# Optimization experiments

Hardware: AMD Instinct MI355X
Metric: run time of the kernel (lower is better)

Reference implementation:

```python
import jax, jax.numpy as jnp
import numpy as np

B, S, H = 2, 2048, 2048      # batch, seq_len, hidden_size
E, K, I = 64, 8, 768         # num_experts, top_k, moe_intermediate_size


def setup_inputs() -> dict:
    key = jax.random.key(0)
    k0, k1, k2, k3, k4 = jax.random.split(key, 5)
    hidden_states = jax.random.normal(k0, (B, S, H), dtype=jnp.float32)
    gate_weight = jax.random.normal(k1, (E, H), dtype=jnp.float32) * 0.02   # router
    w_gate = jax.random.normal(k2, (E, H, I), dtype=jnp.float32) * 0.02    # gate_proj
    w_up = jax.random.normal(k3, (E, H, I), dtype=jnp.float32) * 0.02      # up_proj
    w_down = jax.random.normal(k4, (E, I, H), dtype=jnp.float32) * 0.02    # down_proj
    return {"hidden_states": hidden_states, "gate_weight": gate_weight,
            "w_gate": w_gate, "w_up": w_up, "w_down": w_down}


def _moe_forward(hidden_states, gate_weight, w_gate, w_up, w_down):
    b, s, h = hidden_states.shape
    x = hidden_states.reshape(-1, h)                       # [T, H]
    # ---- router: linear + softmax + top-k + renormalize (fp32, like original) ----
    logits = x.astype(jnp.float32) @ gate_weight.astype(jnp.float32).T  # [T, E]
    scores = jax.nn.softmax(logits, axis=-1)
    topk_w, topk_idx = jax.lax.top_k(scores, K)            # [T, K]
    topk_w = topk_w / jnp.sum(topk_w, axis=-1, keepdims=True)
    # ---- dispatch: replicate each token K times, sort rows by expert id ----
    flat_ids = topk_idx.reshape(-1)                        # [T*K]
    expanded = jnp.repeat(x, K, axis=0)                    # [T*K, H]
    order = jnp.argsort(flat_ids)                          # group rows by expert
    sorted_tokens = expanded[order]                        # [T*K, H], expert-contiguous
    group_sizes = jnp.zeros((E,), jnp.int32).at[flat_ids].add(1)
    # ---- grouped-GEMM expert FFN: down(silu(gate(x)) * up(x)) ----
    g = jax.lax.ragged_dot(sorted_tokens, w_gate, group_sizes)   # [T*K, I]
    u = jax.lax.ragged_dot(sorted_tokens, w_up, group_sizes)     # [T*K, I]
    out = jax.lax.ragged_dot(jax.nn.silu(g) * u, w_down, group_sizes)  # [T*K, H]
    # ---- unshuffle + weighted combine over the K experts per token ----
    inv = jnp.argsort(order)
    outs = out[inv].reshape(-1, K, h)                      # [T, K, H]
    y = jnp.sum(outs * topk_w[:, :, None], axis=1)         # [T, H]
    return y.reshape(b, s, h)


def reference(hidden_states, gate_weight, w_gate, w_up, w_down):
    return _moe_forward(hidden_states, gate_weight, w_gate, w_up, w_down)
```

## Files before the change

### kernel.cpp

```cpp
#include <hip/hip_runtime.h>
#include <math.h>
#include <stdint.h>

constexpr int Bc = 2, Sc = 2048, Hc = 2048, Ec = 64, Kc = 8, Ic = 768;
constexpr int Tc  = Bc * Sc;
constexpr int TKc = Tc * Kc;

__global__ __launch_bounds__(256) void router_topk(
    const float* __restrict__ x, const float* __restrict__ gw,
    int* __restrict__ topk_idx, float* __restrict__ topk_w,
    int* __restrict__ counts)
{
    __shared__ float xs[Hc];
    __shared__ float lg[Ec];
    const int t   = blockIdx.x;
    const int tid = threadIdx.x;

    {
        const float4* src = (const float4*)(x + (size_t)t * Hc);
        float4* dst = (float4*)xs;
        dst[tid * 2]     = src[tid * 2];
        dst[tid * 2 + 1] = src[tid * 2 + 1];
    }
    __syncthreads();

    const int wave = tid >> 6, lane = tid & 63;
    for (int j = 0; j < 16; ++j) {
        const int e = wave * 16 + j;
        const float* gr = gw + (size_t)e * Hc;
        float p = 0.f;
        for (int i = lane; i < Hc; i += 64) p += xs[i] * gr[i];
        for (int off = 32; off; off >>= 1) p += __shfl_down(p, off);
        if (lane == 0) lg[e] = p;
    }
    __syncthreads();

    if (tid < 64) {
        float v = lg[lane];
        int   id = lane;
        float sval[8]; int sid[8];
        for (int k = 0; k < 8; ++k) {
            float bv = v; int bi = id;
            for (int off = 32; off; off >>= 1) {
                float ov = __shfl_down(bv, off);
                int   oi = __shfl_down(bi, off);
                if (ov > bv || (ov == bv && oi < bi)) { bv = ov; bi = oi; }
            }
            bv = __shfl(bv, 0); bi = __shfl(bi, 0);
            sval[k] = bv; sid[k] = bi;
            if (id == bi) v = -INFINITY;
        }
        if (lane == 0) {
            float m = sval[0], s = 0.f, w[8];
            for (int k = 0; k < 8; ++k) { w[k] = expf(sval[k] - m); s += w[k]; }
            const float inv = 1.f / s;
            for (int k = 0; k < 8; ++k) {
                topk_idx[t * 8 + k] = sid[k];
                topk_w[t * 8 + k]   = w[k] * inv;
                atomicAdd(&counts[sid[k]], 1);
            }
        }
    }
}

__global__ void prefix_scan(const int* __restrict__ counts, int* __restrict__ offsets)
{
    if (threadIdx.x == 0 && blockIdx.x == 0) {
        int s = 0;
        for (int e = 0; e < Ec; ++e) { offsets[e] = s; s += counts[e]; }
        offsets[Ec] = s;
    }
}

__global__ __launch_bounds__(256) void scatter_rows(
    const int* __restrict__ topk_idx, const int* __restrict__ offsets,
    int* __restrict__ cursor, int* __restrict__ rowtok)
{
    const int idx = blockIdx.x * 256 + threadIdx.x;
    if (idx < TKc) {
        const int e   = topk_idx[idx];
        const int pos = offsets[e] + atomicAdd(&cursor[e], 1);
        rowtok[pos] = idx;
    }
}

__global__ __launch_bounds__(256) void gemm_act(
    const float* __restrict__ x, const float* __restrict__ wg,
    const float* __restrict__ wu, const int* __restrict__ offsets,
    const int* __restrict__ rowtok, float* __restrict__ act)
{
    __shared__ float As[64][17];
    __shared__ float Bg[16][68];
    __shared__ float Bu[16][68];

    const int e    = blockIdx.y;
    const int base = offsets[e];
    const int M    = offsets[e + 1] - base;
    const int row0 = blockIdx.z * 64;
    if (row0 >= M) return;
    const int n0  = blockIdx.x * 64;
    const int tid = threadIdx.x;

    const int ar = tid >> 2, aq = tid & 3;
    const bool avalid = (row0 + ar) < M;
    const int tok = avalid ? (rowtok[base + row0 + ar] >> 3) : 0;
    const float* arow = x + (size_t)tok * Hc + aq * 4;

    const int bk = tid >> 4, bq = tid & 15;
    const float* wg_base = wg + (size_t)e * Hc * Ic + n0;
    const float* wu_base = wu + (size_t)e * Hc * Ic + n0;

    const int tr = tid >> 4, tc = tid & 15;
    float accg[4][4] = {}, accu[4][4] = {};

    for (int h0 = 0; h0 < Hc; h0 += 16) {
        float4 av = make_float4(0.f, 0.f, 0.f, 0.f);
        if (avalid) av = *(const float4*)(arow + h0);
        As[ar][aq * 4 + 0] = av.x; As[ar][aq * 4 + 1] = av.y;
        As[ar][aq * 4 + 2] = av.z; As[ar][aq * 4 + 3] = av.w;

        const float4 gv = *(const float4*)(wg_base + (size_t)(h0 + bk) * Ic + bq * 4);
        const float4 uv = *(const float4*)(wu_base + (size_t)(h0 + bk) * Ic + bq * 4);
        Bg[bk][bq * 4 + 0] = gv.x; Bg[bk][bq * 4 + 1] = gv.y;
        Bg[bk][bq * 4 + 2] = gv.z; Bg[bk][bq * 4 + 3] = gv.w;
        Bu[bk][bq * 4 + 0] = uv.x; Bu[bk][bq * 4 + 1] = uv.y;
        Bu[bk][bq * 4 + 2] = uv.z; Bu[bk][bq * 4 + 3] = uv.w;
        __syncthreads();

        #pragma unroll
        for (int kk = 0; kk < 16; ++kk) {
            float a[4], bg[4], bu[4];
            #pragma unroll
            for (int i2 = 0; i2 < 4; ++i2) a[i2] = As[tr * 4 + i2][kk];
            #pragma unroll
            for (int j = 0; j < 4; ++j) { bg[j] = Bg[kk][tc * 4 + j]; bu[j] = Bu[kk][tc * 4 + j]; }
            #pragma unroll
            for (int i2 = 0; i2 < 4; ++i2)
                #pragma unroll
                for (int j = 0; j < 4; ++j) {
                    accg[i2][j] += a[i2] * bg[j];
                    accu[i2][j] += a[i2] * bu[j];
                }
        }
        __syncthreads();
    }

    #pragma unroll
    for (int i2 = 0; i2 < 4; ++i2) {
        const int r = tr * 4 + i2;
        if (row0 + r < M) {
            float* orow = act + (size_t)(base + row0 + r) * Ic + n0 + tc * 4;
            #pragma unroll
            for (int j = 0; j < 4; ++j) {
                const float g = accg[i2][j], u = accu[i2][j];
                const float s = g / (1.f + expf(-g));
                orow[j] = s * u;
            }
        }
    }
}

__global__ __launch_bounds__(256) void gemm_down(
    const float* __restrict__ act, const float* __restrict__ wd,
    const int* __restrict__ offsets, const int* __restrict__ rowtok,
    const float* __restrict__ topk_w, float* __restrict__ out)
{
    __shared__ float As[64][17];
    __shared__ float Bs[16][68];

    const int e    = blockIdx.y;
    const int base = offsets[e];
    const int M    = offsets[e + 1] - base;
    const int row0 = blockIdx.z * 64;
    if (row0 >= M) return;
    const int n0  = blockIdx.x * 64;
    const int tid = threadIdx.x;

    const int ar = tid >> 2, aq = tid & 3;
    const bool avalid = (row0 + ar) < M;
    const float* arow = act + (size_t)(base + row0 + ar) * Ic + aq * 4;

    const int bk = tid >> 4, bq = tid & 15;
    const float* wd_base = wd + (size_t)e * Ic * Hc + n0;

    const int tr = tid >> 4, tc = tid & 15;
    float acc[4][4] = {};

    for (int i0 = 0; i0 < Ic; i0 += 16) {
        float4 av = make_float4(0.f, 0.f, 0.f, 0.f);
        if (avalid) av = *(const float4*)(arow + i0);
        As[ar][aq * 4 + 0] = av.x; As[ar][aq * 4 + 1] = av.y;
        As[ar][aq * 4 + 2] = av.z; As[ar][aq * 4 + 3] = av.w;

        const float4 bv = *(const float4*)(wd_base + (size_t)(i0 + bk) * Hc + bq * 4);
        Bs[bk][bq * 4 + 0] = bv.x; Bs[bk][bq * 4 + 1] = bv.y;
        Bs[bk][bq * 4 + 2] = bv.z; Bs[bk][bq * 4 + 3] = bv.w;
        __syncthreads();

        #pragma unroll
        for (int kk = 0; kk < 16; ++kk) {
            float a[4], b[4];
            #pragma unroll
            for (int i2 = 0; i2 < 4; ++i2) a[i2] = As[tr * 4 + i2][kk];
            #pragma unroll
            for (int j = 0; j < 4; ++j) b[j] = Bs[kk][tc * 4 + j];
            #pragma unroll
            for (int i2 = 0; i2 < 4; ++i2)
                #pragma unroll
                for (int j = 0; j < 4; ++j) acc[i2][j] += a[i2] * b[j];
        }
        __syncthreads();
    }

    #pragma unroll
    for (int i2 = 0; i2 < 4; ++i2) {
        const int r = tr * 4 + i2;
        if (row0 + r < M) {
            const int idx = rowtok[base + row0 + r];
            const int t   = idx >> 3;
            const float w = topk_w[idx];
            float* orow = out + (size_t)t * Hc + n0 + tc * 4;
            #pragma unroll
            for (int j = 0; j < 4; ++j) atomicAdd(&orow[j], w * acc[i2][j]);
        }
    }
}

extern "C" void kernel_launch(void* const* d_in, const int* in_sizes, int n_in,
                              void* d_out, int out_size, void* d_ws, size_t ws_size,
                              hipStream_t stream)
{
    const float* x  = (const float*)d_in[0];
    const float* gw = (const float*)d_in[1];
    const float* wg = (const float*)d_in[2];
    const float* wu = (const float*)d_in[3];
    const float* wd = (const float*)d_in[4];
    float* out = (float*)d_out;

    int*   topk_idx = (int*)d_ws;
    float* topk_w   = (float*)(topk_idx + TKc);
    int*   counts   = (int*)(topk_w + TKc);
    int*   offsets  = counts + Ec;
    int*   cursor   = offsets + Ec + 1;
    int*   rowtok   = cursor + Ec;
    float* act      = (float*)((((uintptr_t)(rowtok + TKc)) + 255) & ~(uintptr_t)255);

    hipMemsetAsync(counts, 0, (size_t)(3 * Ec + 1) * sizeof(int), stream);
    hipMemsetAsync(out, 0, (size_t)out_size * sizeof(float), stream);

    router_topk<<<Tc, 256, 0, stream>>>(x, gw, topk_idx, topk_w, counts);
    prefix_scan<<<1, 64, 0, stream>>>(counts, offsets);
    scatter_rows<<<TKc / 256, 256, 0, stream>>>(topk_idx, offsets, cursor, rowtok);
    gemm_act<<<dim3(Ic / 64, Ec, 64), 256, 0, stream>>>(x, wg, wu, offsets, rowtok, act);
    gemm_down<<<dim3(Hc / 64, Ec, 64), 256, 0, stream>>>(act, wd, offsets, rowtok, topk_w, out);
}
```

Baseline: 5.996 ms.

## Run expert GEMMs on bf16 MFMA with hi/lo split emulating fp32

Replaces the scalar-FMA fp32 tiled expert GEMMs with MFMA 16x16x32 bf16 kernels. Each fp32 operand is split into bf16 hi and lo parts, and three MFMAs per tile recover near-fp32 accuracy. Tiles grow to 128x128 and 128x256, LDS is XOR-swizzled, global loads are register double-buffered, and the intermediate activation is stored as a bf16 hi/lo pair. The aim is to move the compute-bound FFN onto the matrix cores, at the cost of on-the-fly weight conversion in every block and a small loss of precision versus true fp32.

Measured after the change: 8.624 ms. 1.44x slower.

```diff
diff --git a/kernel.cpp b/kernel.cpp
--- a/kernel.cpp
+++ b/kernel.cpp
@@ -5,6 +5,31 @@
 constexpr int Bc = 2, Sc = 2048, Hc = 2048, Ec = 64, Kc = 8, Ic = 768;
 constexpr int Tc  = Bc * Sc;
 constexpr int TKc = Tc * Kc;
+
+typedef __attribute__((ext_vector_type(8))) short          bf16x8;
+typedef __attribute__((ext_vector_type(4))) short          s16x4;
+typedef __attribute__((ext_vector_type(8))) unsigned short u16x8;
+typedef __attribute__((ext_vector_type(4))) float          f32x4;
+
+#define SWZ(b) ((b) ^ ((((b) >> 6) & 7) << 4))
+
+__device__ __forceinline__ unsigned short bf_hi(float f) {
+    unsigned u = __float_as_uint(f);
+    u += 0x7fffu + ((u >> 16) & 1u);
+    return (unsigned short)(u >> 16);
+}
+__device__ __forceinline__ void bf_split(float f, short& h, short& l) {
+    unsigned short hb = bf_hi(f);
+    float rem = f - __uint_as_float((unsigned)hb << 16);
+    h = (short)hb;
+    l = (short)bf_hi(rem);
+}
+__device__ __forceinline__ float fc(const float4& v, int j) {
+    switch (j) { case 0: return v.x; case 1: return v.y; case 2: return v.z; default: return v.w; }
+}
+__device__ __forceinline__ f32x4 mma16(bf16x8 a, bf16x8 b, f32x4 c) {
+    return __builtin_amdgcn_mfma_f32_16x16x32_bf16(a, b, c, 0, 0, 0);
+}
 
 __global__ __launch_bounds__(256) void router_topk(
     const float* __restrict__ x, const float* __restrict__ gw,
@@ -84,144 +109,280 @@
     }
 }
 
-__global__ __launch_bounds__(256) void gemm_act(
+__global__ __launch_bounds__(256, 2) void gemm_act(
     const float* __restrict__ x, const float* __restrict__ wg,
     const float* __restrict__ wu, const int* __restrict__ offsets,
-    const int* __restrict__ rowtok, float* __restrict__ act)
-{
-    __shared__ float As[64][17];
-    __shared__ float Bg[16][68];
-    __shared__ float Bu[16][68];
-
-    const int e    = blockIdx.y;
+    const int* __restrict__ rowtok,
+    unsigned short* __restrict__ act_hi, unsigned short* __restrict__ act_lo)
+{
+    __shared__ __align__(16) short Ah[128*32], Al[128*32];
+    __shared__ __align__(16) short Gh[128*32], Gl[128*32];
+    __shared__ __align__(16) short Uh[128*32], Ul[128*32];
+
+    const int e    = blockIdx.z;
     const int base = offsets[e];
     const int M    = offsets[e + 1] - base;
-    const int row0 = blockIdx.z * 64;
+    const int row0 = blockIdx.x * 128;
     if (row0 >= M) return;
-    const int n0  = blockIdx.x * 64;
+    const int n0  = blockIdx.y * 128;
     const int tid = threadIdx.x;
 
-    const int ar = tid >> 2, aq = tid & 3;
-    const bool avalid = (row0 + ar) < M;
-    const int tok = avalid ? (rowtok[base + row0 + ar] >> 3) : 0;
-    const float* arow = x + (size_t)tok * Hc + aq * 4;
-
-    const int bk = tid >> 4, bq = tid & 15;
-    const float* wg_base = wg + (size_t)e * Hc * Ic + n0;
-    const float* wu_base = wu + (size_t)e * Hc * Ic + n0;
-
-    const int tr = tid >> 4, tc = tid & 15;
-    float accg[4][4] = {}, accu[4][4] = {};
-
-    for (int h0 = 0; h0 < Hc; h0 += 16) {
-        float4 av = make_float4(0.f, 0.f, 0.f, 0.f);
-        if (avalid) av = *(const float4*)(arow + h0);
-        As[ar][aq * 4 + 0] = av.x; As[ar][aq * 4 + 1] = av.y;
-        As[ar][aq * 4 + 2] = av.z; As[ar][aq * 4 + 3] = av.w;
-
-        const float4 gv = *(const float4*)(wg_base + (size_t)(h0 + bk) * Ic + bq * 4);
-        const float4 uv = *(const float4*)(wu_base + (size_t)(h0 + bk) * Ic + bq * 4);
-        Bg[bk][bq * 4 + 0] = gv.x; Bg[bk][bq * 4 + 1] = gv.y;
-        Bg[bk][bq * 4 + 2] = gv.z; Bg[bk][bq * 4 + 3] = gv.w;
-        Bu[bk][bq * 4 + 0] = uv.x; Bu[bk][bq * 4 + 1] = uv.y;
-        Bu[bk][bq * 4 + 2] = uv.z; Bu[bk][bq * 4 + 3] = uv.w;
+    const int ar = tid >> 1;
+    const int ak = (tid & 1) * 16;
+    int ridx = base + row0 + ar;
+    if (ridx > TKc - 1) ridx = TKc - 1;
+    const int tok = rowtok[ridx] >> 3;
+    const float* aptr = x + (size_t)tok * Hc + ak;
+
+    const int bq = (tid >> 3) * 4;
+    const int bk = (tid & 7) * 4;
+    const float* gptr = wg + (size_t)e * Hc * Ic + (size_t)bk * Ic + (n0 + bq);
+    const float* uptr = wu + (size_t)e * Hc * Ic + (size_t)bk * Ic + (n0 + bq);
+
+    const int lane = tid & 63, wave = tid >> 6;
+    const int wm = wave >> 1, wn = wave & 1;
+    const int l15 = lane & 15, lk = lane >> 4;
+
+    int aoff[4], boff[4];
+    #pragma unroll
+    for (int m = 0; m < 4; ++m) aoff[m] = SWZ((wm*64 + m*16 + l15) * 64 + lk*16);
+    #pragma unroll
+    for (int n = 0; n < 4; ++n) boff[n] = SWZ((wn*64 + n*16 + l15) * 64 + lk*16);
+
+    f32x4 accg[4][4] = {}, accu[4][4] = {};
+
+    float4 ra[4], rg[4], ru[4];
+    #pragma unroll
+    for (int i = 0; i < 4; ++i) ra[i] = *(const float4*)(aptr + i*4);
+    #pragma unroll
+    for (int i = 0; i < 4; ++i) rg[i] = *(const float4*)(gptr + (size_t)i * Ic);
+    #pragma unroll
+    for (int i = 0; i < 4; ++i) ru[i] = *(const float4*)(uptr + (size_t)i * Ic);
+
+    for (int h0 = 0; h0 < Hc; h0 += 32) {
         __syncthreads();
 
-        #pragma unroll
-        for (int kk = 0; kk < 16; ++kk) {
-            float a[4], bg[4], bu[4];
-            #pragma unroll
-            for (int i2 = 0; i2 < 4; ++i2) a[i2] = As[tr * 4 + i2][kk];
-            #pragma unroll
-            for (int j = 0; j < 4; ++j) { bg[j] = Bg[kk][tc * 4 + j]; bu[j] = Bu[kk][tc * 4 + j]; }
-            #pragma unroll
-            for (int i2 = 0; i2 < 4; ++i2)
+        {
+            const int b0 = ar*64 + ak*2;
+            #pragma unroll
+            for (int q = 0; q < 2; ++q) {
+                bf16x8 vh, vl;
                 #pragma unroll
-                for (int j = 0; j < 4; ++j) {
-                    accg[i2][j] += a[i2] * bg[j];
-                    accu[i2][j] += a[i2] * bu[j];
+                for (int i = 0; i < 2; ++i)
+                    #pragma unroll
+                    for (int j = 0; j < 4; ++j) {
+                        short h, l; bf_split(fc(ra[q*2 + i], j), h, l);
+                        vh[i*4 + j] = h; vl[i*4 + j] = l;
+                    }
+                *(bf16x8*)((char*)Ah + SWZ(b0 + q*16)) = vh;
+                *(bf16x8*)((char*)Al + SWZ(b0 + q*16)) = vl;
+            }
+        }
+        #pragma unroll
+        for (int j = 0; j < 4; ++j) {
+            const int b = (bq + j)*64 + bk*2;
+            s16x4 gh, gl, uh, ul;
+            #pragma unroll
+            for (int i = 0; i < 4; ++i) {
+                short h, l;
+                bf_split(fc(rg[i], j), h, l); gh[i] = h; gl[i] = l;
+                bf_split(fc(ru[i], j), h, l); uh[i] = h; ul[i] = l;
+            }
+            *(s16x4*)((char*)Gh + SWZ(b)) = gh;
+            *(s16x4*)((char*)Gl + SWZ(b)) = gl;
+            *(s16x4*)((char*)Uh + SWZ(b)) = uh;
+            *(s16x4*)((char*)Ul + SWZ(b)) = ul;
+        }
+
+        if (h0 + 32 < Hc) {
+            #pragma unroll
+            for (int i = 0; i < 4; ++i) ra[i] = *(const float4*)(aptr + (h0 + 32) + i*4);
+            #pragma unroll
+            for (int i = 0; i < 4; ++i) rg[i] = *(const float4*)(gptr + (size_t)(h0 + 32 + i) * Ic);
+            #pragma unroll
+            for (int i = 0; i < 4; ++i) ru[i] = *(const float4*)(uptr + (size_t)(h0 + 32 + i) * Ic);
+        }
+
+        __syncthreads();
+
+        bf16x8 fah[4], fal[4];
+        #pragma unroll
+        for (int m = 0; m < 4; ++m) {
+            fah[m] = *(const bf16x8*)((const char*)Ah + aoff[m]);
+            fal[m] = *(const bf16x8*)((const char*)Al + aoff[m]);
+        }
+        #pragma unroll
+        for (int n = 0; n < 4; ++n) {
+            bf16x8 bh = *(const bf16x8*)((const char*)Gh + boff[n]);
+            bf16x8 bl = *(const bf16x8*)((const char*)Gl + boff[n]);
+            #pragma unroll
+            for (int m = 0; m < 4; ++m) {
+                accg[m][n] = mma16(fah[m], bh, accg[m][n]);
+                accg[m][n] = mma16(fal[m], bh, accg[m][n]);
+                accg[m][n] = mma16(fah[m], bl, accg[m][n]);
+            }
+            bh = *(const bf16x8*)((const char*)Uh + boff[n]);
+            bl = *(const bf16x8*)((const char*)Ul + boff[n]);
+            #pragma unroll
+            for (int m = 0; m < 4; ++m) {
+                accu[m][n] = mma16(fah[m], bh, accu[m][n]);
+                accu[m][n] = mma16(fal[m], bh, accu[m][n]);
+                accu[m][n] = mma16(fah[m], bl, accu[m][n]);
+            }
+        }
+    }
+
+    #pragma unroll
+    for (int m = 0; m < 4; ++m) {
+        #pragma unroll
+        for (int r = 0; r < 4; ++r) {
+            const int rl = wm*64 + m*16 + lk*4 + r;
+            if (row0 + rl < M) {
+                unsigned short* oh = act_hi + (size_t)(base + row0 + rl) * Ic + n0;
+                unsigned short* ol = act_lo + (size_t)(base + row0 + rl) * Ic + n0;
+                #pragma unroll
+                for (int n = 0; n < 4; ++n) {
+                    const int c = wn*64 + n*16 + l15;
+                    const float g = accg[m][n][r];
+                    const float u = accu[m][n][r];
+                    const float s = (g / (1.f + expf(-g))) * u;
+                    short h, l; bf_split(s, h, l);
+                    oh[c] = (unsigned short)h;
+                    ol[c] = (unsigned short)l;
                 }
-        }
-        __syncthreads();
-    }
-
-    #pragma unroll
-    for (int i2 = 0; i2 < 4; ++i2) {
-        const int r = tr * 4 + i2;
-        if (row0 + r < M) {
-            float* orow = act + (size_t)(base + row0 + r) * Ic + n0 + tc * 4;
-            #pragma unroll
-            for (int j = 0; j < 4; ++j) {
-                const float g = accg[i2][j], u = accu[i2][j];
-                const float s = g / (1.f + expf(-g));
-                orow[j] = s * u;
-            }
-        }
-    }
-}
-
-__global__ __launch_bounds__(256) void gemm_down(
-    const float* __restrict__ act, const float* __restrict__ wd,
-    const int* __restrict__ offsets, const int* __restrict__ rowtok,
-    const float* __restrict__ topk_w, float* __restrict__ out)
-{
-    __shared__ float As[64][17];
-    __shared__ float Bs[16][68];
-
-    const int e    = blockIdx.y;
+            }
+        }
+    }
+}
+
+__global__ __launch_bounds__(256, 2) void gemm_down(
+    const unsigned short* __restrict__ act_hi, const unsigned short* __restrict__ act_lo,
+    const float* __restrict__ wd, const int* __restrict__ offsets,
+    const int* __restrict__ rowtok, const float* __restrict__ topk_w,
+    float* __restrict__ out)
+{
+    __shared__ __align__(16) short Ah[128*32], Al[128*32];
+    __shared__ __align__(16) short Bh[256*32], Bl[256*32];
+
+    const int e    = blockIdx.z;
     const int base = offsets[e];
     const int M    = offsets[e + 1] - base;
-    const int row0 = blockIdx.z * 64;
+    const int row0 = blockIdx.x * 128;
     if (row0 >= M) return;
-    const int n0  = blockIdx.x * 64;
+    const int n0  = blockIdx.y * 256;
     const int tid = threadIdx.x;
 
-    const int ar = tid >> 2, aq = tid & 3;
-    const bool avalid = (row0 + ar) < M;
-    const float* arow = act + (size_t)(base + row0 + ar) * Ic + aq * 4;
-
-    const int bk = tid >> 4, bq = tid & 15;
-    const float* wd_base = wd + (size_t)e * Ic * Hc + n0;
-
-    const int tr = tid >> 4, tc = tid & 15;
-    float acc[4][4] = {};
-
-    for (int i0 = 0; i0 < Ic; i0 += 16) {
-        float4 av = make_float4(0.f, 0.f, 0.f, 0.f);
-        if (avalid) av = *(const float4*)(arow + i0);
-        As[ar][aq * 4 + 0] = av.x; As[ar][aq * 4 + 1] = av.y;
-        As[ar][aq * 4 + 2] = av.z; As[ar][aq * 4 + 3] = av.w;
-
-        const float4 bv = *(const float4*)(wd_base + (size_t)(i0 + bk) * Hc + bq * 4);
-        Bs[bk][bq * 4 + 0] = bv.x; Bs[bk][bq * 4 + 1] = bv.y;
-        Bs[bk][bq * 4 + 2] = bv.z; Bs[bk][bq * 4 + 3] = bv.w;
+    const int ar = tid >> 1;
+    const int ak = (tid & 1) * 16;
+    int ridx = base + row0 + ar;
+    if (ridx > TKc - 1) ridx = TKc - 1;
+    const unsigned short* ahp = act_hi + (size_t)ridx * Ic + ak;
+    const unsigned short* alp = act_lo + (size_t)ridx * Ic + ak;
+
+    const int bq = (tid >> 3) * 4;
+    const int bk = (tid & 7) * 4;
+    const float* bptr = wd + (size_t)e * Ic * Hc + (size_t)bk * Hc + (n0 + bq);
+
+    const int lane = tid & 63, wave = tid >> 6;
+    const int wm = wave >> 1, wn = wave & 1;
+    const int l15 = lane & 15, lk = lane >> 4;
+
+    int aoff[4], boff[8];
+    #pragma unroll
+    for (int m = 0; m < 4; ++m) aoff[m] = SWZ((wm*64 + m*16 + l15) * 64 + lk*16);
+    #pragma unroll
+    for (int n = 0; n < 8; ++n) boff[n] = SWZ((wn*128 + n*16 + l15) * 64 + lk*16);
+
+    f32x4 acc[4][8] = {};
+
+    u16x8 rah[2], ral[2];
+    float4 rb[2][4];
+    #pragma unroll
+    for (int q = 0; q < 2; ++q) {
+        rah[q] = *(const u16x8*)(ahp + q*8);
+        ral[q] = *(const u16x8*)(alp + q*8);
+    }
+    #pragma unroll
+    for (int p = 0; p < 2; ++p)
+        #pragma unroll
+        for (int i = 0; i < 4; ++i)
+            rb[p][i] = *(const float4*)(bptr + (size_t)i * Hc + p*128);
+
+    for (int i0 = 0; i0 < Ic; i0 += 32) {
         __syncthreads();
 
-        #pragma unroll
-        for (int kk = 0; kk < 16; ++kk) {
-            float a[4], b[4];
-            #pragma unroll
-            for (int i2 = 0; i2 < 4; ++i2) a[i2] = As[tr * 4 + i2][kk];
-            #pragma unroll
-            for (int j = 0; j < 4; ++j) b[j] = Bs[kk][tc * 4 + j];
-            #pragma unroll
-            for (int i2 = 0; i2 < 4; ++i2)
+        {
+            const int b0 = ar*64 + ak*2;
+            *(u16x8*)((char*)Ah + SWZ(b0))      = rah[0];
+            *(u16x8*)((char*)Ah + SWZ(b0 + 16)) = rah[1];
+            *(u16x8*)((char*)Al + SWZ(b0))      = ral[0];
+            *(u16x8*)((char*)Al + SWZ(b0 + 16)) = ral[1];
+        }
+        #pragma unroll
+        for (int p = 0; p < 2; ++p)
+            #pragma unroll
+            for (int j = 0; j < 4; ++j) {
+                const int b = (bq + p*128 + j)*64 + bk*2;
+                s16x4 vh, vl;
                 #pragma unroll
-                for (int j = 0; j < 4; ++j) acc[i2][j] += a[i2] * b[j];
-        }
+                for (int i = 0; i < 4; ++i) {
+                    short h, l; bf_split(fc(rb[p][i], j), h, l);
+                    vh[i] = h; vl[i] = l;
+                }
+                *(s16x4*)((char*)Bh + SWZ(b)) = vh;
+                *(s16x4*)((char*)Bl + SWZ(b)) = vl;
+            }
+
+        if (i0 + 32 < Ic) {
+            #pragma unroll
+            for (int q = 0; q < 2; ++q) {
+                rah[q] = *(const u16x8*)(ahp + (i0 + 32) + q*8);
+                ral[q] = *(const u16x8*)(alp + (i0 + 32) + q*8);
+            }
+            #pragma unroll
+            for (int p = 0; p < 2; ++p)
+                #pragma unroll
+                for (int i = 0; i < 4; ++i)
+                    rb[p][i] = *(const float4*)(bptr + (size_t)(i0 + 32 + i) * Hc + p*128);
+        }
+
         __syncthreads();
-    }
-
-    #pragma unroll
-    for (int i2 = 0; i2 < 4; ++i2) {
-        const int r = tr * 4 + i2;
-        if (row0 + r < M) {
-            const int idx = rowtok[base + row0 + r];
-            const int t   = idx >> 3;
-            const float w = topk_w[idx];
-            float* orow = out + (size_t)t * Hc + n0 + tc * 4;
-            #pragma unroll
-            for (int j = 0; j < 4; ++j) atomicAdd(&orow[j], w * acc[i2][j]);
+
+        bf16x8 fah[4], fal[4];
+        #pragma unroll
+        for (int m = 0; m < 4; ++m) {
+            fah[m] = *(const bf16x8*)((const char*)Ah + aoff[m]);
+            fal[m] = *(const bf16x8*)((const char*)Al + aoff[m]);
+        }
+        #pragma unroll
+        for (int n = 0; n < 8; ++n) {
+            bf16x8 bh = *(const bf16x8*)((const char*)Bh + boff[n]);
+            bf16x8 bl = *(const bf16x8*)((const char*)Bl + boff[n]);
+            #pragma unroll
+            for (int m = 0; m < 4; ++m) {
+                acc[m][n] = mma16(fah[m], bh, acc[m][n]);
+                acc[m][n] = mma16(fal[m], bh, acc[m][n]);
+                acc[m][n] = mma16(fah[m], bl, acc[m][n]);
+            }
+        }
+    }
+
+    #pragma unroll
+    for (int m = 0; m < 4; ++m) {
+        #pragma unroll
+        for (int r = 0; r < 4; ++r) {
+            const int rl = wm*64 + m*16 + lk*4 + r;
+            if (row0 + rl < M) {
+                const int idx = rowtok[base + row0 + rl];
+                const int t   = idx >> 3;
+                const float w = topk_w[idx];
+                float* orow = out + (size_t)t * Hc + n0;
+                #pragma unroll
+                for (int n = 0; n < 8; ++n) {
+                    const int c = wn*128 + n*16 + l15;
+                    atomicAdd(&orow[c], w * acc[m][n][r]);
+                }
+            }
         }
     }
 }
@@ -238,19 +399,20 @@
     float* out = (float*)d_out;
 
     int*   topk_idx = (int*)d_ws;
-    float* topk_w   = (float*)(topk_idx + TKc);
-    int*   counts   = (int*)(topk_w + TKc);
+    float* topk_wv  = (float*)(topk_idx + TKc);
+    int*   counts   = (int*)(topk_wv + TKc);
     int*   offsets  = counts + Ec;
     int*   cursor   = offsets + Ec + 1;
     int*   rowtok   = cursor + Ec;
-    float* act      = (float*)((((uintptr_t)(rowtok + TKc)) + 255) & ~(uintptr_t)255);
+    unsigned short* act_hi = (unsigned short*)((((uintptr_t)(rowtok + TKc)) + 255) & ~(uintptr_t)255);
+    unsigned short* act_lo = act_hi + (size_t)TKc * Ic;
 
     hipMemsetAsync(counts, 0, (size_t)(3 * Ec + 1) * sizeof(int), stream);
     hipMemsetAsync(out, 0, (size_t)out_size * sizeof(float), stream);
 
-    router_topk<<<Tc, 256, 0, stream>>>(x, gw, topk_idx, topk_w, counts);
+    router_topk<<<Tc, 256, 0, stream>>>(x, gw, topk_idx, topk_wv, counts);
     prefix_scan<<<1, 64, 0, stream>>>(counts, offsets);
     scatter_rows<<<TKc / 256, 256, 0, stream>>>(topk_idx, offsets, cursor, rowtok);
-    gemm_act<<<dim3(Ic / 64, Ec, 64), 256, 0, stream>>>(x, wg, wu, offsets, rowtok, act);
-    gemm_down<<<dim3(Hc / 64, Ec, 64), 256, 0, stream>>>(act, wd, offsets, rowtok, topk_w, out);
-}
+    gemm_act<<<dim3(32, Ic / 128, Ec), 256, 0, stream>>>(x, wg, wu, offsets, rowtok, act_hi, act_lo);
+    gemm_down<<<dim3(32, Hc / 256, Ec), 256, 0, stream>>>(act_hi, act_lo, wd, offsets, rowtok, topk_wv, out);
+}
```
